# Performance work log

Measured on AMD Instinct MI355X. Metric: run time of the kernel, lower is better.

The kernel has to match this reference:

```python
import jax, jax.numpy as jnp
import numpy as np

EPS = 1e-5

def layer_norm(x, w):
    mu = jnp.mean(x, axis=-1, keepdims=True)
    var = jnp.mean((x - mu) ** 2, axis=-1, keepdims=True)
    return (x - mu) * jax.lax.rsqrt(var + EPS) * w

def timestep_embedding(t, dim=256, max_period=10000.0):
    half = dim // 2
    freqs = jnp.exp(-np.log(max_period) * jnp.arange(half, dtype=jnp.float32) / half)
    args = t[:, None].astype(jnp.float32) * freqs[None]
    return jnp.concatenate([jnp.cos(args), jnp.sin(args)], axis=-1)  # (B, dim)


def setup_inputs() -> dict:
    key = jax.random.key(0)
    ks = jax.random.split(key, 16)
    B, S, D, H, L, V, C, F = 2, 1024, 768, 12, 12, 50258, 768, 256
    MLP = 4 * D
    w = 0.02  # init scale for weights
    return {
        "indices": jax.random.randint(ks[0], (B, S), 0, V, dtype=jnp.int32),
        "sigma": jax.random.uniform(ks[1], (B,), dtype=jnp.float32),
        "embed": jax.random.normal(ks[2], (V, D), jnp.float32) * w,
        "t_w1": jax.random.normal(ks[3], (C, F), jnp.float32) * w,
        "t_b1": jnp.zeros((C,), jnp.float32),
        "t_w2": jax.random.normal(ks[4], (C, C), jnp.float32) * w,
        "t_b2": jnp.zeros((C,), jnp.float32),
        "norm1_w": jnp.ones((L, D), jnp.float32),
        "qkv_w": jax.random.normal(ks[5], (L, 3 * D, D), jnp.float32) * w,
        "out_w": jax.random.normal(ks[6], (L, D, D), jnp.float32) * w,
        "norm2_w": jnp.ones((L, D), jnp.float32),
        "mlp_w1": jax.random.normal(ks[7], (L, MLP, D), jnp.float32) * w,
        "mlp_b1": jnp.zeros((L, MLP), jnp.float32),
        "mlp_w2": jax.random.normal(ks[8], (L, D, MLP), jnp.float32) * w,
        "mlp_b2": jnp.zeros((L, D), jnp.float32),
        "ada_w": jax.random.normal(ks[9], (L, 6 * D, C), jnp.float32) * w,
        "ada_b": jnp.zeros((L, 6 * D), jnp.float32),
        "normf_w": jnp.ones((D,), jnp.float32),
        "lin_w": jax.random.normal(ks[10], (V, D), jnp.float32) * w,
        "lin_b": jnp.zeros((V,), jnp.float32),
        "adaf_w": jax.random.normal(ks[11], (2 * D, C), jnp.float32) * w,
        "adaf_b": jnp.zeros((2 * D,), jnp.float32),
    }


def reference(indices, sigma, embed, t_w1, t_b1, t_w2, t_b2, norm1_w, qkv_w,
              out_w, norm2_w, mlp_w1, mlp_b1, mlp_w2, mlp_b2, ada_w, ada_b,
              normf_w, lin_w, lin_b, adaf_w, adaf_b):
    B, S = indices.shape
    D = embed.shape[1]
    L = qkv_w.shape[0]
    H = 12
    dh = D // H
    scale = 1.0 / np.sqrt(dh)

    x = embed[indices]  # (B, S, D)
    # conditioning: c = silu(MLP(sinusoidal(sigma)))
    tf = timestep_embedding(sigma)
    temb = jax.nn.silu(tf @ t_w1.T + t_b1) @ t_w2.T + t_b2
    c = jax.nn.silu(temb)  # (B, C)

    # NOTE: rotary cos/sin are computed but never applied in the original block.
    for l in range(L):
        ada = (c @ ada_w[l].T + ada_b[l]).reshape(B, 6, 1, D)
        sh_msa, sc_msa, g_msa = ada[:, 0], ada[:, 1], ada[:, 2]  # (B, 1, D)
        sh_mlp, sc_mlp, g_mlp = ada[:, 3], ada[:, 4], ada[:, 5]

        xm = layer_norm(x, norm1_w[l]) * (1 + sc_msa) + sh_msa
        qkv = (xm @ qkv_w[l].T).reshape(B, S, 3, H, dh)
        q, k, v = qkv[:, :, 0], qkv[:, :, 1], qkv[:, :, 2]  # (B, S, H, dh)
        attn = jnp.einsum('bqhd,bkhd->bhqk', q, k) * scale
        attn = jax.nn.softmax(attn, axis=-1)
        o = jnp.einsum('bhqk,bkhd->bqhd', attn, v).reshape(B, S, D)
        x = x + g_msa * (o @ out_w[l].T)

        xm = layer_norm(x, norm2_w[l]) * (1 + sc_mlp) + sh_mlp
        h = jax.nn.gelu(xm @ mlp_w1[l].T + mlp_b1[l], approximate=True)
        x = x + g_mlp * (h @ mlp_w2[l].T + mlp_b2[l])

    ada = (c @ adaf_w.T + adaf_b).reshape(B, 2, 1, D)
    shift, sc = ada[:, 0], ada[:, 1]
    xm = layer_norm(x, normf_w) * (1 + sc) + shift
    return xm @ lin_w.T + lin_b  # (B, S, V) log-scores
```

## Files before the change

### kernel.cpp

```cpp
#include <hip/hip_runtime.h>
#include <hip/hip_bf16.h>
#include <math.h>
#include <stdint.h>

typedef __hip_bfloat16 bf16;
typedef __attribute__((ext_vector_type(8))) short bf16x8;
typedef __attribute__((ext_vector_type(4))) float f32x4;

#define DEV_INLINE __device__ __forceinline__

DEV_INLINE float wred_sum(float v) {
    #pragma unroll
    for (int o = 32; o > 0; o >>= 1) v += __shfl_xor(v, o);
    return v;
}
DEV_INLINE float red16_max(float v) {
    v = fmaxf(v, __shfl_xor(v, 1)); v = fmaxf(v, __shfl_xor(v, 2));
    v = fmaxf(v, __shfl_xor(v, 4)); v = fmaxf(v, __shfl_xor(v, 8));
    return v;
}
DEV_INLINE float red16_sum(float v) {
    v += __shfl_xor(v, 1); v += __shfl_xor(v, 2);
    v += __shfl_xor(v, 4); v += __shfl_xor(v, 8);
    return v;
}
DEV_INLINE float gelu_tanh(float v) {
    float t = tanhf(0.7978845608028654f * (v + 0.044715f * v * v * v));
    return 0.5f * v * (1.f + t);
}
DEV_INLINE float silu(float v) { return v / (1.f + expf(-v)); }
DEV_INLINE short f2bs(float f) { bf16 h = __float2bfloat16(f); short s; __builtin_memcpy(&s, &h, 2); return s; }

typedef const __attribute__((address_space(1))) uint32_t* gptr_t;
typedef __attribute__((address_space(3))) uint32_t* lptr_t;

DEV_INLINE void gload_lds16(const bf16* gp, bf16* lp) {
    __builtin_amdgcn_global_load_lds((gptr_t)gp, (lptr_t)lp, 16, 0, 0);
}

#define WAITBAR12() asm volatile("s_waitcnt vmcnt(12)\ns_barrier" ::: "memory")
#define WAITBAR8()  asm volatile("s_waitcnt vmcnt(8)\ns_barrier" ::: "memory")
#define WAITBAR4()  asm volatile("s_waitcnt vmcnt(4)\ns_barrier" ::: "memory")
#define WAITBAR0()  asm volatile("s_waitcnt vmcnt(0)\ns_barrier" ::: "memory")

DEV_INLINE int xcd_swz(int wg, int nwg) {
    int q = nwg >> 3, r = nwg & 7;
    int xcd = wg & 7, pos = wg >> 3;
    return (xcd < r ? xcd * (q + 1) : r * (q + 1) + (xcd - r) * q) + pos;
}

__global__ void cvt_bf16(const float* __restrict__ in, bf16* __restrict__ out, long n) {
    long i = ((long)blockIdx.x * blockDim.x + threadIdx.x) * 8;
    if (i >= n) return;
    float4 a = *(const float4*)(in + i);
    float4 b = *(const float4*)(in + i + 4);
    bf16x8 v;
    v[0] = f2bs(a.x); v[1] = f2bs(a.y); v[2] = f2bs(a.z); v[3] = f2bs(a.w);
    v[4] = f2bs(b.x); v[5] = f2bs(b.y); v[6] = f2bs(b.z); v[7] = f2bs(b.w);
    *(bf16x8*)(out + i) = v;
}

__global__ void embed_gather(const int* __restrict__ idx,
                             const float* __restrict__ embed,
                             float* __restrict__ x) {
    int i = blockIdx.x * blockDim.x + threadIdx.x;
    int m = i / 192, d4 = i % 192;
    ((float4*)x)[(size_t)m * 192 + d4] =
        ((const float4*)embed)[(size_t)idx[m] * 192 + d4];
}

__global__ void tstep_embed(const float* __restrict__ sigma, float* __restrict__ tf) {
    int t = threadIdx.x;
    int b = t >> 7, i = t & 127;
    float freq = expf(-9.210340371976184f * (float)i / 128.f);
    float a = sigma[b] * freq;
    tf[b * 256 + i]       = cosf(a);
    tf[b * 256 + 128 + i] = sinf(a);
}

template <int ACT>
__global__ void gemm_rowvec(const float* __restrict__ A, const float* __restrict__ W,
                            const float* __restrict__ bias, float* __restrict__ C,
                            int M, int N, int K) {
    int wid  = (int)((blockIdx.x * (size_t)blockDim.x + threadIdx.x) >> 6);
    int lane = threadIdx.x & 63;
    if (wid >= M * N) return;
    int m = wid / N, n = wid % N;
    const float* a = A + (size_t)m * K;
    const float* w = W + (size_t)n * K;
    float s = 0.f;
    for (int k = lane; k < K; k += 64) s = fmaf(a[k], w[k], s);
    s = wred_sum(s);
    if (lane == 0) {
        if (bias) s += bias[n];
        if (ACT == 2) s = silu(s);
        C[wid] = s;
    }
}

__global__ void ada_all(const float* __restrict__ c, const float* __restrict__ ada_w,
                        const float* __restrict__ ada_b, float* __restrict__ out) {
    const int C = 768, SIXD = 4608, B = 2;
    int wid  = (int)((blockIdx.x * (size_t)blockDim.x + threadIdx.x) >> 6);
    int lane = threadIdx.x & 63;
    if (wid >= 12 * B * SIXD) return;
    int j = wid % SIXD;
    int lb = wid / SIXD;
    int b = lb % B, l = lb / B;
    const float* a = c + (size_t)b * C;
    const float* w = ada_w + ((size_t)l * SIXD + j) * C;
    float s = 0.f;
    for (int k = lane; k < C; k += 64) s = fmaf(a[k], w[k], s);
    s = wred_sum(s);
    if (lane == 0) out[wid] = s + ada_b[l * SIXD + j];
}

__global__ __launch_bounds__(256) void ln_mod(const float* __restrict__ x,
                                              const float* __restrict__ w,
                                              const float* __restrict__ sc,
                                              const float* __restrict__ sh,
                                              int bstride,
                                              bf16* __restrict__ out) {
    int r = blockIdx.x;
    int b = r >> 10;
    const float* xr = x + (size_t)r * 768;
    int tid = threadIdx.x, lane = tid & 63, wv = tid >> 6;
    float v0 = xr[tid], v1 = xr[tid + 256], v2 = xr[tid + 512];
    __shared__ float redA[4], redB[4];
    float s = wred_sum(v0 + v1 + v2);
    if (lane == 0) redA[wv] = s;
    __syncthreads();
    float mu = (redA[0] + redA[1] + redA[2] + redA[3]) * (1.f / 768.f);
    float d0 = v0 - mu, d1 = v1 - mu, d2 = v2 - mu;
    float vs = wred_sum(d0 * d0 + d1 * d1 + d2 * d2);
    if (lane == 0) redB[wv] = vs;
    __syncthreads();
    float var  = (redB[0] + redB[1] + redB[2] + redB[3]) * (1.f / 768.f);
    float rstd = rsqrtf(var + 1e-5f);
    const float* scb = sc + (size_t)b * bstride;
    const float* shb = sh + (size_t)b * bstride;
    bf16* outr = out + (size_t)r * 768;
    outr[tid]       = __float2bfloat16(d0 * rstd * w[tid]       * (1.f + scb[tid])       + shb[tid]);
    outr[tid + 256] = __float2bfloat16(d1 * rstd * w[tid + 256] * (1.f + scb[tid + 256]) + shb[tid + 256]);
    outr[tid + 512] = __float2bfloat16(d2 * rstd * w[tid + 512] * (1.f + scb[tid + 512]) + shb[tid + 512]);
}

template <int NPART>
__global__ __launch_bounds__(256) void ln_mod_red(float* __restrict__ x,
                                                  const float* __restrict__ part,
                                                  const float* __restrict__ bias,
                                                  const float* __restrict__ gate,
                                                  int gst,
                                                  const float* __restrict__ w,
                                                  const float* __restrict__ sc,
                                                  const float* __restrict__ sh,
                                                  int bstride,
                                                  bf16* __restrict__ out) {
    const size_t PST = (size_t)2048 * 768;
    int r = blockIdx.x;
    int b = r >> 10;
    float* xr = x + (size_t)r * 768;
    int tid = threadIdx.x, lane = tid & 63, wv = tid >> 6;

    float v[3];
    #pragma unroll
    for (int e = 0; e < 3; e++) {
        int d = tid + e * 256;
        float s0 = 0.f;
        #pragma unroll
        for (int p = 0; p < NPART; p++) s0 += part[(size_t)p * PST + (size_t)r * 768 + d];
        if (bias) s0 += bias[d];
        v[e] = xr[d] + gate[b * gst + d] * s0;
        xr[d] = v[e];
    }

    __shared__ float redA[4], redB[4];
    float s = wred_sum(v[0] + v[1] + v[2]);
    if (lane == 0) redA[wv] = s;
    __syncthreads();
    float mu = (redA[0] + redA[1] + redA[2] + redA[3]) * (1.f / 768.f);
    float d0 = v[0] - mu, d1 = v[1] - mu, d2 = v[2] - mu;
    float vs = wred_sum(d0 * d0 + d1 * d1 + d2 * d2);
    if (lane == 0) redB[wv] = vs;
    __syncthreads();
    float var  = (redB[0] + redB[1] + redB[2] + redB[3]) * (1.f / 768.f);
    float rstd = rsqrtf(var + 1e-5f);
    const float* scb = sc + (size_t)b * bstride;
    const float* shb = sh + (size_t)b * bstride;
    bf16* outr = out + (size_t)r * 768;
    outr[tid]       = __float2bfloat16(d0 * rstd * w[tid]       * (1.f + scb[tid])       + shb[tid]);
    outr[tid + 256] = __float2bfloat16(d1 * rstd * w[tid + 256] * (1.f + scb[tid + 256]) + shb[tid + 256]);
    outr[tid + 512] = __float2bfloat16(d2 * rstd * w[tid + 512] * (1.f + scb[tid + 512]) + shb[tid + 512]);
}

template <int ACT, int OMODE, int SK>
__global__ __launch_bounds__(256) void gemm_mfma(const bf16* __restrict__ A,
                                                 const bf16* __restrict__ W,
                                                 const float* __restrict__ bias,
                                                 void* __restrict__ Cout,
                                                 bf16* __restrict__ vtout,
                                                 int M, int N, int K) {
    __shared__ __align__(16) bf16 SHB[6 * 128 * 32];
    int tid = threadIdx.x;
    int w = tid >> 6, l = tid & 63;
    int l16 = l & 15, g = l >> 4;
    int wgid = xcd_swz(blockIdx.x, gridDim.x);
    int MT = M >> 7;
    int nt = gridDim.x / (MT * SK);
    int m0 = (wgid % MT) * 128;
    int n  = (wgid / MT) % nt;
    int s  = wgid / (MT * nt);
    int n0 = n * 128;
    int kb = K / SK;
    int k0 = s * kb;
    int wr = (w >> 1) * 64, wc = (w & 1) * 64;

    f32x4 acc[4][4];
    f32x4 zero4 = {0.f, 0.f, 0.f, 0.f};
    #pragma unroll
    for (int i = 0; i < 4; i++)
        #pragma unroll
        for (int j = 0; j < 4; j++) acc[i][j] = zero4;

    int srow = w * 32 + (l >> 2);
    int scol = ((l & 3) ^ ((l >> 3) & 3)) * 8;
    const bf16* gA0 = A + (size_t)(m0 + srow) * K + k0 + scol;
    const bf16* gA1 = gA0 + (size_t)16 * K;
    int nr0 = n0 + srow;      if (nr0 > N - 1) nr0 = N - 1;
    int nr1 = n0 + srow + 16; if (nr1 > N - 1) nr1 = N - 1;
    const bf16* gW0 = W + (size_t)nr0 * K + k0 + scol;
    const bf16* gW1 = W + (size_t)nr1 * K + k0 + scol;
    int ldsA0 = (w * 32) * 32, ldsA1 = (w * 32 + 16) * 32;
    int sA = (g ^ ((l16 >> 1) & 3)) * 8;

    auto SAp = [&](int bufi) { return &SHB[bufi * 4096]; };
    auto SWp = [&](int bufi) { return &SHB[(3 + bufi) * 4096]; };

    int KT = kb >> 5;
    gload_lds16(gA0 + 0, SAp(0) + ldsA0);
    gload_lds16(gA1 + 0, SAp(0) + ldsA1);
    gload_lds16(gW0 + 0, SWp(0) + ldsA0);
    gload_lds16(gW1 + 0, SWp(0) + ldsA1);
    if (KT > 1) {
        gload_lds16(gA0 + 32, SAp(1) + ldsA0);
        gload_lds16(gA1 + 32, SAp(1) + ldsA1);
        gload_lds16(gW0 + 32, SWp(1) + ldsA0);
        gload_lds16(gW1 + 32, SWp(1) + ldsA1);
    }

    for (int k = 0; k < KT; ++k) {
        if (k == KT - 1) { WAITBAR0(); } else { WAITBAR4(); }
        if (k + 2 < KT) {
            int bufi = (k + 2) % 3, kk = (k + 2) * 32;
            gload_lds16(gA0 + kk, SAp(bufi) + ldsA0);
            gload_lds16(gA1 + kk, SAp(bufi) + ldsA1);
            gload_lds16(gW0 + kk, SWp(bufi) + ldsA0);
            gload_lds16(gW1 + kk, SWp(bufi) + ldsA1);
        }
        int cbuf = k % 3;
        const bf16* sa = SAp(cbuf);
        const bf16* sw = SWp(cbuf);
        bf16x8 af[4], bfr[4];
        #pragma unroll
        for (int mi = 0; mi < 4; mi++)
            af[mi] = *(const bf16x8*)&sa[(wr + mi * 16 + l16) * 32 + sA];
        #pragma unroll
        for (int ni = 0; ni < 4; ni++)
            bfr[ni] = *(const bf16x8*)&sw[(wc + ni * 16 + l16) * 32 + sA];
        #pragma unroll
        for (int mi = 0; mi < 4; mi++)
            #pragma unroll
            for (int ni = 0; ni < 4; ni++)
                acc[mi][ni] = __builtin_amdgcn_mfma_f32_16x16x32_bf16(
                    af[mi], bfr[ni], acc[mi][ni], 0, 0, 0);
    }

    if (OMODE == 3 && n0 >= 1536) {
        #pragma unroll
        for (int ni = 0; ni < 4; ni++) {
            int cv = n0 + wc + ni * 16 + l16 - 1536;
            int h = cv >> 6, d = cv & 63;
            #pragma unroll
            for (int mi = 0; mi < 4; mi++) {
                int row = m0 + wr + mi * 16 + g * 4;
                int b = row >> 10, ss = row & 1023;
                short4 pk;
                pk.x = f2bs(acc[mi][ni][0]); pk.y = f2bs(acc[mi][ni][1]);
                pk.z = f2bs(acc[mi][ni][2]); pk.w = f2bs(acc[mi][ni][3]);
                *(short4*)&vtout[(((size_t)(b * 12 + h) * 64 + d)) * 1024 + ss] = pk;
            }
        }
        return;
    }
    float* pout = (OMODE == 4) ? (float*)Cout + (size_t)s * M * N : (float*)Cout;
    #pragma unroll
    for (int ni = 0; ni < 4; ni++) {
        int col = n0 + wc + ni * 16 + l16;
        if (col >= N) continue;
        float bv = (OMODE != 4 && bias) ? bias[col] : 0.f;
        #pragma unroll
        for (int mi = 0; mi < 4; mi++) {
            #pragma unroll
            for (int jj = 0; jj < 4; jj++) {
                int row = m0 + wr + mi * 16 + g * 4 + jj;
                float v = acc[mi][ni][jj] + bv;
                if (ACT == 1) v = gelu_tanh(v);
                if (OMODE == 1 || OMODE == 3) {
                    ((bf16*)Cout)[(size_t)row * N + col] = __float2bfloat16(v);
                } else {
                    pout[(size_t)row * N + col] = v;
                }
            }
        }
    }
}

__global__ __launch_bounds__(512) void gemm_vocab(const bf16* __restrict__ A,
                                                  const bf16* __restrict__ W,
                                                  const float* __restrict__ bias,
                                                  float* __restrict__ Cout,
                                                  int M, int N, int K) {
    __shared__ __align__(16) bf16 SHB[65536];
    int tid = threadIdx.x;
    int w = tid >> 6, l = tid & 63;
    int l16 = l & 15, g = l >> 4;
    int wm = w >> 2, wn = w & 3;
    int wgid = xcd_swz(blockIdx.x, gridDim.x);
    int MT = M >> 8;
    int m0 = (wgid % MT) * 256;
    int n0 = (wgid / MT) * 256;

    f32x4 acc[8][4];
    f32x4 zero4 = {0.f, 0.f, 0.f, 0.f};
    #pragma unroll
    for (int i = 0; i < 8; i++)
        #pragma unroll
        for (int j = 0; j < 4; j++) acc[i][j] = zero4;

    int srow = w * 16 + (l >> 2);
    int scol = ((l & 3) ^ ((l >> 3) & 3)) * 8;
    const bf16* gA0 = A + (size_t)(m0 + srow) * K + scol;
    const bf16* gA1 = gA0 + (size_t)128 * K;
    int nb0 = n0 + srow;       if (nb0 > N - 1) nb0 = N - 1;
    int nb1 = n0 + 128 + srow; if (nb1 > N - 1) nb1 = N - 1;
    const bf16* gB0 = W + (size_t)nb0 * K + scol;
    const bf16* gB1 = W + (size_t)nb1 * K + scol;
    int ldw = (w * 16) * 32;
    int sA = (g ^ ((l16 >> 1) & 3)) * 8;

    auto SAp = [&](int bufi) { return &SHB[bufi * 8192]; };
    auto SBp = [&](int bufi) { return &SHB[32768 + bufi * 8192]; };

    auto STAGE = [&](int t) {
        int bufi = t & 3, kk = t * 32;
        gload_lds16(gA0 + kk, SAp(bufi) + ldw);
        gload_lds16(gA1 + kk, SAp(bufi) + 4096 + ldw);
        gload_lds16(gB0 + kk, SBp(bufi) + ldw);
        gload_lds16(gB1 + kk, SBp(bufi) + 4096 + ldw);
    };

    int KT = K >> 5;
    STAGE(0); STAGE(1); STAGE(2);

    for (int k = 0; k < KT; ++k) {
        if (k + 3 < KT) STAGE(k + 3);
        int rem = KT - 1 - k; if (rem > 3) rem = 3;
        if (rem == 3) { WAITBAR12(); }
        else if (rem == 2) { WAITBAR8(); }
        else if (rem == 1) { WAITBAR4(); }
        else { WAITBAR0(); }
        int cbuf = k & 3;
        const bf16* sa = SAp(cbuf);
        const bf16* sb = SBp(cbuf);
        bf16x8 af[8], bfr[4];
        #pragma unroll
        for (int mi = 0; mi < 8; mi++)
            af[mi] = *(const bf16x8*)&sa[(wm * 128 + mi * 16 + l16) * 32 + sA];
        #pragma unroll
        for (int ni = 0; ni < 4; ni++)
            bfr[ni] = *(const bf16x8*)&sb[(wn * 64 + ni * 16 + l16) * 32 + sA];
        #pragma unroll
        for (int mi = 0; mi < 8; mi++)
            #pragma unroll
            for (int ni = 0; ni < 4; ni++)
                acc[mi][ni] = __builtin_amdgcn_mfma_f32_16x16x32_bf16(
                    af[mi], bfr[ni], acc[mi][ni], 0, 0, 0);
    }

    float* Lf = (float*)SHB;
    #pragma unroll
    for (int h = 0; h < 4; ++h) {
        __syncthreads();
        if (wm == (h >> 1)) {
            int mi0 = (h & 1) * 4;
            #pragma unroll
            for (int ni = 0; ni < 4; ni++) {
                int lc = wn * 64 + ni * 16 + l16;
                int colg = n0 + lc;
                float bv = (bias && colg < N) ? bias[colg] : 0.f;
                #pragma unroll
                for (int mi2 = 0; mi2 < 4; mi2++) {
                    int lr = mi2 * 16 + g * 4;
                    #pragma unroll
                    for (int jj = 0; jj < 4; jj++)
                        Lf[(lr + jj) * 260 + lc] = acc[mi0 + mi2][ni][jj] + bv;
                }
            }
        }
        __syncthreads();
        #pragma unroll
        for (int pass = 0; pass < 8; ++pass) {
            int row = pass * 8 + (tid >> 6);
            int c4  = (tid & 63) * 4;
            const float* src = &Lf[row * 260 + c4];
            float* dst = Cout + (size_t)(m0 + h * 64 + row) * N + n0 + c4;
            int col = n0 + c4;
            if (col + 3 < N) {
                *(float2*)dst       = *(const float2*)src;
                *(float2*)(dst + 2) = *(const float2*)(src + 2);
            } else {
                #pragma unroll
                for (int e = 0; e < 4; ++e)
                    if (col + e < N) dst[e] = src[e];
            }
        }
    }
}

__global__ __launch_bounds__(256) void attn_mfma(const bf16* __restrict__ qkv,
                                                 const bf16* __restrict__ vt,
                                                 bf16* __restrict__ ao) {
    const int S = 1024, C3 = 2304;
    int wgid = xcd_swz(blockIdx.x, gridDim.x);
    int bh = wgid >> 4, b = bh / 12, h = bh % 12;
    int q0 = (wgid & 15) * 64;
    int tid = threadIdx.x, w = tid >> 6, l = tid & 63;
    int l16 = l & 15, g = l >> 4;

    __shared__ __align__(16) bf16 Ks[3][64 * 64];
    __shared__ __align__(16) bf16 Vs[3][64 * 64];
    __shared__ __align__(16) bf16 Ps[4][16 * 72];

    const size_t qbase = ((size_t)(b * S + q0 + w * 16 + l16)) * C3 + h * 64;
    bf16x8 qf[2];
    qf[0] = *(const bf16x8*)&qkv[qbase + g * 8];
    qf[1] = *(const bf16x8*)&qkv[qbase + 32 + g * 8];

    f32x4 o_acc[4];
    f32x4 zero4 = {0.f, 0.f, 0.f, 0.f};
    #pragma unroll
    for (int ni = 0; ni < 4; ni++) o_acc[ni] = zero4;
    float mrow[4] = {-1e30f, -1e30f, -1e30f, -1e30f};
    float lrow[4] = {0.f, 0.f, 0.f, 0.f};
    const float cscale = 0.125f * 1.44269504088896f;

    int sr0 = w * 16 + (l >> 3);
    int sr1 = sr0 + 8;
    int cb  = (l & 7) * 16;
    int sc0 = (cb ^ ((sr0 & 7) << 4)) >> 1;
    int sc1 = (cb ^ ((sr1 & 7) << 4)) >> 1;
    const bf16* gk0 = qkv + ((size_t)(b * S) + sr0) * C3 + 768 + h * 64 + sc0;
    const bf16* gk1 = qkv + ((size_t)(b * S) + sr1) * C3 + 768 + h * 64 + sc1;
    const bf16* gv0 = vt + ((size_t)bh * 64 + sr0) * 1024 + sc0;
    const bf16* gv1 = vt + ((size_t)bh * 64 + sr1) * 1024 + sc1;
    int ldk0 = (w * 16) * 64, ldk1 = (w * 16 + 8) * 64;

    auto STAGEKV = [&](int t, int bufi) {
        gload_lds16(gk0 + (size_t)(t * 64) * C3, &Ks[bufi][ldk0]);
        gload_lds16(gk1 + (size_t)(t * 64) * C3, &Ks[bufi][ldk1]);
        gload_lds16(gv0 + t * 64, &Vs[bufi][ldk0]);
        gload_lds16(gv1 + t * 64, &Vs[bufi][ldk1]);
    };

    STAGEKV(0, 0);
    STAGEKV(1, 1);

    for (int it = 0; it < 16; ++it) {
        if (it == 15) { WAITBAR0(); } else { WAITBAR4(); }
        if (it + 2 < 16) STAGEKV(it + 2, (it + 2) % 3);
        int cur = it % 3;

        f32x4 sfrag[4];
        #pragma unroll
        for (int kf = 0; kf < 4; kf++) {
            sfrag[kf] = zero4;
            int key = kf * 16 + l16;
            #pragma unroll
            for (int kc = 0; kc < 2; kc++) {
                int byteoff = key * 128 + (((kc * 32 + g * 8) * 2) ^ ((key & 7) << 4));
                bf16x8 kb = *(const bf16x8*)((const char*)Ks[cur] + byteoff);
                sfrag[kf] = __builtin_amdgcn_mfma_f32_16x16x32_bf16(qf[kc], kb, sfrag[kf], 0, 0, 0);
            }
        }

        float pv[4][4];
        #pragma unroll
        for (int j = 0; j < 4; j++) {
            float t0 = sfrag[0][j] * cscale, t1 = sfrag[1][j] * cscale;
            float t2 = sfrag[2][j] * cscale, t3 = sfrag[3][j] * cscale;
            float mx = fmaxf(fmaxf(t0, t1), fmaxf(t2, t3));
            mx = red16_max(mx);
            float mnew = fmaxf(mrow[j], mx);
            float r = exp2f(mrow[j] - mnew);
            mrow[j] = mnew;
            float p0 = exp2f(t0 - mnew), p1 = exp2f(t1 - mnew);
            float p2 = exp2f(t2 - mnew), p3 = exp2f(t3 - mnew);
            pv[0][j] = p0; pv[1][j] = p1; pv[2][j] = p2; pv[3][j] = p3;
            float ps = red16_sum(p0 + p1 + p2 + p3);
            lrow[j] = lrow[j] * r + ps;
            #pragma unroll
            for (int ni = 0; ni < 4; ni++) o_acc[ni][j] *= r;
        }

        #pragma unroll
        for (int kf = 0; kf < 4; kf++)
            #pragma unroll
            for (int j = 0; j < 4; j++)
                Ps[w][(g * 4 + j) * 72 + kf * 16 + l16] = __float2bfloat16(pv[kf][j]);

        #pragma unroll
        for (int kc = 0; kc < 2; kc++) {
            bf16x8 pa = *(const bf16x8*)&Ps[w][l16 * 72 + kc * 32 + g * 8];
            #pragma unroll
            for (int ni = 0; ni < 4; ni++) {
                int d = ni * 16 + l16;
                int byteoff = d * 128 + (((kc * 32 + g * 8) * 2) ^ ((d & 7) << 4));
                bf16x8 vb = *(const bf16x8*)((const char*)Vs[cur] + byteoff);
                o_acc[ni] = __builtin_amdgcn_mfma_f32_16x16x32_bf16(pa, vb, o_acc[ni], 0, 0, 0);
            }
        }
    }

    float linv[4];
    #pragma unroll
    for (int j = 0; j < 4; j++) linv[j] = 1.f / lrow[j];
    #pragma unroll
    for (int ni = 0; ni < 4; ni++) {
        #pragma unroll
        for (int jj = 0; jj < 4; jj++) {
            int row = q0 + w * 16 + g * 4 + jj;
            ao[((size_t)(b * S + row)) * 768 + h * 64 + ni * 16 + l16] =
                __float2bfloat16(o_acc[ni][jj] * linv[jj]);
        }
    }
}

extern "C" void kernel_launch(void* const* d_in, const int* in_sizes, int n_in,
                              void* d_out, int out_size, void* d_ws, size_t ws_size,
                              hipStream_t stream) {
    const int B = 2, S = 1024, D = 768, L = 12, V = 50258, C = 768, F = 256, MLP = 3072;
    const int M = B * S;

    const int*   indices = (const int*)d_in[0];
    const float* sigma   = (const float*)d_in[1];
    const float* embed   = (const float*)d_in[2];
    const float* t_w1    = (const float*)d_in[3];
    const float* t_b1    = (const float*)d_in[4];
    const float* t_w2    = (const float*)d_in[5];
    const float* t_b2    = (const float*)d_in[6];
    const float* norm1_w = (const float*)d_in[7];
    const float* qkv_w   = (const float*)d_in[8];
    const float* out_w   = (const float*)d_in[9];
    const float* norm2_w = (const float*)d_in[10];
    const float* mlp_w1  = (const float*)d_in[11];
    const float* mlp_b1  = (const float*)d_in[12];
    const float* mlp_w2  = (const float*)d_in[13];
    const float* mlp_b2  = (const float*)d_in[14];
    const float* ada_w   = (const float*)d_in[15];
    const float* ada_b   = (const float*)d_in[16];
    const float* normf_w = (const float*)d_in[17];
    const float* lin_w   = (const float*)d_in[18];
    const float* lin_b   = (const float*)d_in[19];
    const float* adaf_w  = (const float*)d_in[20];
    const float* adaf_b  = (const float*)d_in[21];

    char* p = (char*)d_ws;
    auto alloc = [&](size_t bytes) { char* r = p; p += (bytes + 255) & ~(size_t)255; return r; };

    float* x     = (float*)alloc((size_t)M * D * 4);
    bf16*  xm    = (bf16*) alloc((size_t)M * D * 2);
    bf16*  qkvb  = (bf16*) alloc((size_t)M * 3 * D * 2);
    bf16*  aob   = (bf16*) alloc((size_t)M * D * 2);
    bf16*  hbb   = (bf16*) alloc((size_t)M * MLP * 2);
    bf16*  vtb   = (bf16*) alloc((size_t)24 * 64 * 1024 * 2);
    float* partb = (float*)alloc((size_t)4 * M * D * 4);
    bf16*  linb  = (bf16*) alloc((size_t)V * D * 2);
    float* tf    = (float*)alloc((size_t)B * F * 4);
    float* h1    = (float*)alloc((size_t)B * C * 4);
    float* cb    = (float*)alloc((size_t)B * C * 4);
    float* ada   = (float*)alloc((size_t)L * B * 6 * D * 4);
    float* adaf  = (float*)alloc((size_t)B * 2 * D * 4);

    const size_t n_qkvw = (size_t)L * 2304 * 768;
    const size_t n_outw = (size_t)L * 768 * 768;
    const size_t n_w1   = (size_t)L * 3072 * 768;
    const size_t n_w2   = (size_t)L * 768 * 3072;
    const size_t per_layer = (size_t)(2304 + 768 + 3072 + 3072) * 768;
    size_t used = (size_t)(p - (char*)d_ws);
    bool all_w = (ws_size - used) >= ((n_qkvw + n_outw + n_w1 + n_w2) * 2 + 1024);

    bf16 *wqkv, *wout, *ww1, *ww2;
    if (all_w) {
        wqkv = (bf16*)alloc(n_qkvw * 2);
        wout = (bf16*)alloc(n_outw * 2);
        ww1  = (bf16*)alloc(n_w1 * 2);
        ww2  = (bf16*)alloc(n_w2 * 2);
    } else {
        bf16* wl = (bf16*)alloc(per_layer * 2);
        wqkv = wl;
        wout = wqkv + (size_t)2304 * 768;
        ww1  = wout + (size_t)768 * 768;
        ww2  = ww1 + (size_t)3072 * 768;
    }

    auto cgrid = [](long n) { return (unsigned)((n / 8 + 255) / 256); };
    dim3 blk(256);

    embed_gather<<<(M * 192) / 256, blk, 0, stream>>>(indices, embed, x);
    tstep_embed<<<1, blk, 0, stream>>>(sigma, tf);
    gemm_rowvec<2><<<(B * C * 64) / 256, blk, 0, stream>>>(tf, t_w1, t_b1, h1, B, C, F);
    gemm_rowvec<2><<<(B * C * 64) / 256, blk, 0, stream>>>(h1, t_w2, t_b2, cb, B, C, C);
    ada_all<<<(L * B * 6 * D * 64) / 256, blk, 0, stream>>>(cb, ada_w, ada_b, ada);
    gemm_rowvec<0><<<(B * 2 * D * 64) / 256, blk, 0, stream>>>(cb, adaf_w, adaf_b, adaf, B, 2 * D, C);
    cvt_bf16<<<cgrid((long)V * D), blk, 0, stream>>>(lin_w, linb, (long)V * D);
    if (all_w) {
        cvt_bf16<<<cgrid((long)n_qkvw), blk, 0, stream>>>(qkv_w, wqkv, (long)n_qkvw);
        cvt_bf16<<<cgrid((long)n_outw), blk, 0, stream>>>(out_w, wout, (long)n_outw);
        cvt_bf16<<<cgrid((long)n_w1),   blk, 0, stream>>>(mlp_w1, ww1, (long)n_w1);
        cvt_bf16<<<cgrid((long)n_w2),   blk, 0, stream>>>(mlp_w2, ww2, (long)n_w2);
    }

    const int MT = M / 128;
    for (int l = 0; l < L; l++) {
        const float* adaL = ada + (size_t)l * B * 6 * D;
        bf16 *wq, *wo, *w1, *w2;
        if (all_w) {
            wq = wqkv + (size_t)l * 2304 * 768;
            wo = wout + (size_t)l * 768 * 768;
            w1 = ww1 + (size_t)l * 3072 * 768;
            w2 = ww2 + (size_t)l * 768 * 3072;
        } else {
            wq = wqkv; wo = wout; w1 = ww1; w2 = ww2;
            cvt_bf16<<<cgrid((long)2304 * 768), blk, 0, stream>>>(qkv_w + (size_t)l * 2304 * 768, wq, (long)2304 * 768);
            cvt_bf16<<<cgrid((long)768 * 768),  blk, 0, stream>>>(out_w + (size_t)l * 768 * 768,  wo, (long)768 * 768);
            cvt_bf16<<<cgrid((long)3072 * 768), blk, 0, stream>>>(mlp_w1 + (size_t)l * 3072 * 768, w1, (long)3072 * 768);
            cvt_bf16<<<cgrid((long)768 * 3072), blk, 0, stream>>>(mlp_w2 + (size_t)l * 768 * 3072, w2, (long)768 * 3072);
        }

        if (l == 0) {
            ln_mod<<<M, blk, 0, stream>>>(x, norm1_w, adaL + D, adaL, 6 * D, xm);
        } else {
            const float* adaP = ada + (size_t)(l - 1) * B * 6 * D;
            ln_mod_red<4><<<M, blk, 0, stream>>>(
                x, partb, mlp_b2 + (size_t)(l - 1) * D, adaP + 5 * D, 6 * D,
                norm1_w + (size_t)l * D, adaL + D, adaL, 6 * D, xm);
        }

        gemm_mfma<0, 3, 1><<<MT * (2304 / 128), blk, 0, stream>>>(
            xm, wq, nullptr, qkvb, vtb, M, 2304, 768);
        attn_mfma<<<384, blk, 0, stream>>>(qkvb, vtb, aob);
        gemm_mfma<0, 4, 2><<<MT * (768 / 128) * 2, blk, 0, stream>>>(
            aob, wo, nullptr, partb, nullptr, M, 768, 768);
        ln_mod_red<2><<<M, blk, 0, stream>>>(
            x, partb, nullptr, adaL + 2 * D, 6 * D,
            norm2_w + (size_t)l * D, adaL + 4 * D, adaL + 3 * D, 6 * D, xm);

        gemm_mfma<1, 1, 1><<<MT * (3072 / 128), blk, 0, stream>>>(
            xm, w1, mlp_b1 + (size_t)l * MLP, hbb, nullptr, M, 3072, 768);
        gemm_mfma<0, 4, 4><<<MT * (768 / 128) * 4, blk, 0, stream>>>(
            hbb, w2, nullptr, partb, nullptr, M, 768, 3072);
    }

    {
        const float* adaP = ada + (size_t)(L - 1) * B * 6 * D;
        ln_mod_red<4><<<M, blk, 0, stream>>>(
            x, partb, mlp_b2 + (size_t)(L - 1) * D, adaP + 5 * D, 6 * D,
            normf_w, adaf + D, adaf, 2 * D, xm);
    }
    gemm_vocab<<<(M / 256) * ((V + 255) / 256), dim3(512), 0, stream>>>(
        xm, linb, lin_b, (float*)d_out, M, V, 768);
}
```

Measured before the change: 2.089 ms.

## Split GEMM inner loop into two MFMA halves with priority boosts and mid-barrier

Both the generic GEMM and the vocab GEMM now load A fragments in two halves, interleaving LDS reads with MFMA groups. The MFMA groups are wrapped in s_setprio, with an extra s_barrier between halves to keep waves in lockstep, so matrix work overlaps with memory and LDS traffic. The vocab GEMM drops from a 4-stage to a 3-stage LDS pipeline, reducing shared memory and fragment registers to improve occupancy. The tradeoff is less prefetch depth and an extra barrier per k-step.

```diff
diff --git a/kernel.cpp b/kernel.cpp
--- a/kernel.cpp
+++ b/kernel.cpp
@@ -38,8 +38,6 @@
     __builtin_amdgcn_global_load_lds((gptr_t)gp, (lptr_t)lp, 16, 0, 0);
 }
 
-#define WAITBAR12() asm volatile("s_waitcnt vmcnt(12)\ns_barrier" ::: "memory")
-#define WAITBAR8()  asm volatile("s_waitcnt vmcnt(8)\ns_barrier" ::: "memory")
 #define WAITBAR4()  asm volatile("s_waitcnt vmcnt(4)\ns_barrier" ::: "memory")
 #define WAITBAR0()  asm volatile("s_waitcnt vmcnt(0)\ns_barrier" ::: "memory")
 
@@ -249,30 +247,46 @@
     }
 
     for (int k = 0; k < KT; ++k) {
-        if (k == KT - 1) { WAITBAR0(); } else { WAITBAR4(); }
         if (k + 2 < KT) {
             int bufi = (k + 2) % 3, kk = (k + 2) * 32;
             gload_lds16(gA0 + kk, SAp(bufi) + ldsA0);
             gload_lds16(gA1 + kk, SAp(bufi) + ldsA1);
             gload_lds16(gW0 + kk, SWp(bufi) + ldsA0);
             gload_lds16(gW1 + kk, SWp(bufi) + ldsA1);
+            WAITBAR4();
+        } else {
+            WAITBAR0();
         }
         int cbuf = k % 3;
         const bf16* sa = SAp(cbuf);
         const bf16* sw = SWp(cbuf);
-        bf16x8 af[4], bfr[4];
-        #pragma unroll
-        for (int mi = 0; mi < 4; mi++)
-            af[mi] = *(const bf16x8*)&sa[(wr + mi * 16 + l16) * 32 + sA];
+        bf16x8 af[2], bfr[4];
         #pragma unroll
         for (int ni = 0; ni < 4; ni++)
             bfr[ni] = *(const bf16x8*)&sw[(wc + ni * 16 + l16) * 32 + sA];
         #pragma unroll
-        for (int mi = 0; mi < 4; mi++)
+        for (int mi = 0; mi < 2; mi++)
+            af[mi] = *(const bf16x8*)&sa[(wr + mi * 16 + l16) * 32 + sA];
+        __builtin_amdgcn_s_setprio(1);
+        #pragma unroll
+        for (int mi = 0; mi < 2; mi++)
             #pragma unroll
             for (int ni = 0; ni < 4; ni++)
                 acc[mi][ni] = __builtin_amdgcn_mfma_f32_16x16x32_bf16(
                     af[mi], bfr[ni], acc[mi][ni], 0, 0, 0);
+        __builtin_amdgcn_s_setprio(0);
+        __builtin_amdgcn_s_barrier();
+        #pragma unroll
+        for (int mi = 0; mi < 2; mi++)
+            af[mi] = *(const bf16x8*)&sa[(wr + (mi + 2) * 16 + l16) * 32 + sA];
+        __builtin_amdgcn_s_setprio(1);
+        #pragma unroll
+        for (int mi = 0; mi < 2; mi++)
+            #pragma unroll
+            for (int ni = 0; ni < 4; ni++)
+                acc[mi + 2][ni] = __builtin_amdgcn_mfma_f32_16x16x32_bf16(
+                    af[mi], bfr[ni], acc[mi + 2][ni], 0, 0, 0);
+        __builtin_amdgcn_s_setprio(0);
     }
 
     if (OMODE == 3 && n0 >= 1536) {
@@ -320,7 +334,7 @@
                                                   const float* __restrict__ bias,
                                                   float* __restrict__ Cout,
                                                   int M, int N, int K) {
-    __shared__ __align__(16) bf16 SHB[65536];
+    __shared__ __align__(16) bf16 SHB[49152];
     int tid = threadIdx.x;
     int w = tid >> 6, l = tid & 63;
     int l16 = l & 15, g = l >> 4;
@@ -349,10 +363,10 @@
     int sA = (g ^ ((l16 >> 1) & 3)) * 8;
 
     auto SAp = [&](int bufi) { return &SHB[bufi * 8192]; };
-    auto SBp = [&](int bufi) { return &SHB[32768 + bufi * 8192]; };
+    auto SBp = [&](int bufi) { return &SHB[24576 + bufi * 8192]; };
 
     auto STAGE = [&](int t) {
-        int bufi = t & 3, kk = t * 32;
+        int bufi = t % 3, kk = t * 32;
         gload_lds16(gA0 + kk, SAp(bufi) + ldw);
         gload_lds16(gA1 + kk, SAp(bufi) + 4096 + ldw);
         gload_lds16(gB0 + kk, SBp(bufi) + ldw);
@@ -360,31 +374,42 @@
     };
 
     int KT = K >> 5;
-    STAGE(0); STAGE(1); STAGE(2);
+    STAGE(0);
+    if (KT > 1) STAGE(1);
 
     for (int k = 0; k < KT; ++k) {
-        if (k + 3 < KT) STAGE(k + 3);
-        int rem = KT - 1 - k; if (rem > 3) rem = 3;
-        if (rem == 3) { WAITBAR12(); }
-        else if (rem == 2) { WAITBAR8(); }
-        else if (rem == 1) { WAITBAR4(); }
+        if (k + 2 < KT) { STAGE(k + 2); WAITBAR4(); }
         else { WAITBAR0(); }
-        int cbuf = k & 3;
+        int cbuf = k % 3;
         const bf16* sa = SAp(cbuf);
         const bf16* sb = SBp(cbuf);
-        bf16x8 af[8], bfr[4];
-        #pragma unroll
-        for (int mi = 0; mi < 8; mi++)
-            af[mi] = *(const bf16x8*)&sa[(wm * 128 + mi * 16 + l16) * 32 + sA];
+        bf16x8 af[4], bfr[4];
         #pragma unroll
         for (int ni = 0; ni < 4; ni++)
             bfr[ni] = *(const bf16x8*)&sb[(wn * 64 + ni * 16 + l16) * 32 + sA];
         #pragma unroll
-        for (int mi = 0; mi < 8; mi++)
+        for (int mi = 0; mi < 4; mi++)
+            af[mi] = *(const bf16x8*)&sa[(wm * 128 + mi * 16 + l16) * 32 + sA];
+        __builtin_amdgcn_s_setprio(1);
+        #pragma unroll
+        for (int mi = 0; mi < 4; mi++)
             #pragma unroll
             for (int ni = 0; ni < 4; ni++)
                 acc[mi][ni] = __builtin_amdgcn_mfma_f32_16x16x32_bf16(
                     af[mi], bfr[ni], acc[mi][ni], 0, 0, 0);
+        __builtin_amdgcn_s_setprio(0);
+        __builtin_amdgcn_s_barrier();
+        #pragma unroll
+        for (int mi = 0; mi < 4; mi++)
+            af[mi] = *(const bf16x8*)&sa[(wm * 128 + (mi + 4) * 16 + l16) * 32 + sA];
+        __builtin_amdgcn_s_setprio(1);
+        #pragma unroll
+        for (int mi = 0; mi < 4; mi++)
+            #pragma unroll
+            for (int ni = 0; ni < 4; ni++)
+                acc[mi + 4][ni] = __builtin_amdgcn_mfma_f32_16x16x32_bf16(
+                    af[mi], bfr[ni], acc[mi + 4][ni], 0, 0, 0);
+        __builtin_amdgcn_s_setprio(0);
     }
 
     float* Lf = (float*)SHB;
```

Result: slower. 2.169 ms (+3.8%).
